# Kernel tuning notes

Measured on AMD Instinct MI355X. Metric: run time of the kernel, lower is better.

## Reference

```python
import jax, jax.numpy as jnp
import numpy as np

E = 8        # n_experts
K = 2        # top-k
DIM = 1024
HID = 2048   # swiglu hidden; fc1 out = 2*HID
B, T = 4, 2048


def setup_inputs() -> dict:
    key = jax.random.key(0)
    ks = jax.random.split(key, 7)
    s = 0.02
    return {
        "x": jax.random.normal(ks[0], (B, T, DIM), dtype=jnp.float32),
        "router_w": jax.random.normal(ks[1], (E, DIM), dtype=jnp.float32) * s,
        "router_b": jnp.zeros((E,), dtype=jnp.float32),
        "W1": jax.random.normal(ks[2], (E, DIM, 2 * HID), dtype=jnp.float32) * s,
        "b1": jnp.zeros((E, 2 * HID), dtype=jnp.float32),
        "W2": jax.random.normal(ks[3], (E, HID, DIM), dtype=jnp.float32) * s,
        "b2": jnp.zeros((E, DIM), dtype=jnp.float32),
    }


def _swiglu(h):
    h1, h2 = jnp.split(h, 2, axis=-1)
    return jax.nn.silu(h1) * h2


def reference(x, router_w, router_b, W1, b1, W2, b2):
    # Router: logits = Linear(dim, E), temperature = 1.0
    logits = jnp.einsum("btd,ed->bte", x, router_w) + router_b  # [B,T,E]
    topk_val, topk_idx = jax.lax.top_k(logits, K)               # [B,T,K]
    weights = jax.nn.softmax(topk_val, axis=-1)                 # softmax router
    # combine[b,t,e] = sum_k weights[b,t,k] * [topk_idx[b,t,k] == e]
    combine = jnp.sum(jax.nn.one_hot(topk_idx, E, dtype=x.dtype)
                      * weights[..., None], axis=-2)            # [B,T,E]
    out = jnp.zeros_like(x)
    # Fixed small loop over experts (structurally distinct weight slices).
    for e in range(E):
        h = jnp.einsum("btd,dh->bth", x, W1[e]) + b1[e]         # [B,T,2H]
        y = jnp.einsum("bth,hd->btd", _swiglu(h), W2[e]) + b2[e]
        out = out + combine[..., e:e + 1] * y
    return out
```

## Files before the change

### kernel.cpp

```cpp
#include <hip/hip_runtime.h>
#include <stdint.h>

typedef unsigned short u16;

#define E_    8
#define DIM_  1024
#define HID_  2048
#define H2_   4096
#define NTOK  8192
#define SLAB  ((size_t)NTOK * 2 * DIM_)

typedef __attribute__((ext_vector_type(8))) short bf16x8;
typedef __attribute__((ext_vector_type(4))) float f32x4;

__device__ __forceinline__ u16 f2bf(float f) {
  uint32_t u = __builtin_bit_cast(uint32_t, f);
  uint32_t r = (u + 0x7FFFu + ((u >> 16) & 1u)) >> 16;
  return (u16)r;
}
__device__ __forceinline__ float bf2f(u16 u) {
  return __builtin_bit_cast(float, (uint32_t)u << 16);
}

__device__ __forceinline__ void gload16(const void* g, void* l) {
  __builtin_amdgcn_global_load_lds(
      (const __attribute__((address_space(1))) void*)g,
      (__attribute__((address_space(3))) void*)l, 16, 0, 0);
}


__global__ void tconvF(const float* __restrict__ W1, u16* __restrict__ w1t,
                       const float* __restrict__ W2, u16* __restrict__ w2t) {
  __shared__ float t[64][65];
  int b = blockIdx.x;
  const float* src; u16* dst; int R, C, e, bx, by;
  if (b < 8192) {
    e = b >> 10; int rem = b & 1023;
    bx = rem & 63; by = rem >> 6;
    src = W1; dst = w1t; R = DIM_; C = H2_;
  } else {
    int b2 = b - 8192;
    e = b2 >> 9; int rem = b2 & 511;
    bx = rem & 15; by = rem >> 4;
    src = W2; dst = w2t; R = HID_; C = DIM_;
  }
  int r0 = by * 64, c0 = bx * 64;
  const float* s = src + (size_t)e * R * C;
  u16* d = dst + (size_t)e * R * C;
  int tid = threadIdx.x;
  int rr = tid >> 4, cc = (tid & 15) * 4;
#pragma unroll
  for (int p = 0; p < 4; ++p) {
    float4 v = *(const float4*)(s + (size_t)(r0 + p * 16 + rr) * C + c0 + cc);
    t[p * 16 + rr][cc + 0] = v.x; t[p * 16 + rr][cc + 1] = v.y;
    t[p * 16 + rr][cc + 2] = v.z; t[p * 16 + rr][cc + 3] = v.w;
  }
  __syncthreads();
  int cr = tid >> 3, rc = (tid & 7) * 8;
#pragma unroll
  for (int p = 0; p < 2; ++p) {
    union { u16 u[8]; uint4 v; } w;
#pragma unroll
    for (int j = 0; j < 8; ++j) w.u[j] = f2bf(t[rc + j][p * 32 + cr]);
    *(uint4*)(d + (size_t)(c0 + p * 32 + cr) * R + r0 + rc) = w.v;
  }
}


__global__ void routerA(const float* __restrict__ x, const float* __restrict__ rw,
                        const float* __restrict__ rb, u16* __restrict__ xb,
                        int* __restrict__ gcnt, int2* __restrict__ te_l,
                        float2* __restrict__ tw) {
  __shared__ float srw[E_ * DIM_];
  __shared__ float sb[E_];
  __shared__ int   hcnt[E_];

  int tid = threadIdx.x;
  for (int i = tid; i < E_ * DIM_ / 4; i += 256)
    ((float4*)srw)[i] = ((const float4*)rw)[i];
  if (tid < E_) { sb[tid] = rb[tid]; hcnt[tid] = 0; }
  __syncthreads();

  int wid = tid >> 6, lane = tid & 63;
#pragma unroll
  for (int s = 0; s < 2; ++s) {
    int t = blockIdx.x * 8 + wid * 2 + s;
    const float* xt = x + (size_t)t * DIM_;
    float acc[8] = {0.f, 0.f, 0.f, 0.f, 0.f, 0.f, 0.f, 0.f};
#pragma unroll
    for (int it = 0; it < 4; ++it) {
      int d = it * 256 + lane * 4;
      float4 xv = *(const float4*)(xt + d);
      ushort4 xo;
      xo.x = f2bf(xv.x); xo.y = f2bf(xv.y); xo.z = f2bf(xv.z); xo.w = f2bf(xv.w);
      *(ushort4*)(xb + (size_t)t * DIM_ + d) = xo;
#pragma unroll
      for (int e = 0; e < 8; ++e) {
        float4 rv = *(const float4*)(&srw[e * DIM_ + d]);
        acc[e] += xv.x * rv.x + xv.y * rv.y + xv.z * rv.z + xv.w * rv.w;
      }
    }
#pragma unroll
    for (int e = 0; e < 8; ++e)
#pragma unroll
      for (int off = 32; off; off >>= 1)
        acc[e] += __shfl_xor(acc[e], off, 64);
    if (lane == 0) {
      float v[8];
#pragma unroll
      for (int e = 0; e < 8; ++e) v[e] = acc[e] + sb[e];
      int i0 = 0;
#pragma unroll
      for (int e = 1; e < 8; ++e) if (v[e] > v[i0]) i0 = e;
      int i1 = (i0 == 0) ? 1 : 0;
#pragma unroll
      for (int e = 0; e < 8; ++e) if (e != i0 && v[e] > v[i1]) i1 = e;
      float w0 = 1.f / (1.f + expf(v[i1] - v[i0]));
      int l0 = atomicAdd(&hcnt[i0], 1);
      int l1 = atomicAdd(&hcnt[i1], 1);
      te_l[t] = make_int2((i0 << 8) | l0, (i1 << 8) | l1);
      tw[t] = make_float2(w0, 1.f - w0);
    }
  }
  __syncthreads();
  if (tid < E_) gcnt[tid * 1024 + blockIdx.x] = hcnt[tid];
}


__global__ void routerB(const int* __restrict__ gcnt, int* __restrict__ base_blk,
                        int* __restrict__ counts) {
  __shared__ int part[256];
  int tid = threadIdx.x;
#pragma unroll
  for (int e = 0; e < 8; ++e) {
    int4 v = *(const int4*)(gcnt + e * 1024 + tid * 4);
    int s = v.x + v.y + v.z + v.w;
    part[tid] = s;
    __syncthreads();
    for (int off = 1; off < 256; off <<= 1) {
      int o = (tid >= off) ? part[tid - off] : 0;
      __syncthreads();
      part[tid] += o;
      __syncthreads();
    }
    int ex = part[tid] - s;
    int tot = part[255];
    int4 b;
    b.x = ex; b.y = ex + v.x; b.z = ex + v.x + v.y; b.w = ex + v.x + v.y + v.z;
    *(int4*)(base_blk + e * 1024 + tid * 4) = b;
    if (tid == 0) counts[e] = tot;
    __syncthreads();
  }
}


__global__ void routerC(const int2* __restrict__ te_l, const float2* __restrict__ tw,
                        const int* __restrict__ base_blk, int* __restrict__ btok,
                        float* __restrict__ bw, int* __restrict__ tokrec) {
  int t = blockIdx.x * 256 + threadIdx.x;
  int2 r = te_l[t];
  float2 w = tw[t];
  int b = t >> 3;
  int e0 = r.x >> 8, l0 = r.x & 255;
  int e1 = r.y >> 8, l1 = r.y & 255;
  int p0 = base_blk[e0 * 1024 + b] + l0;
  int p1 = base_blk[e1 * 1024 + b] + l1;
  btok[e0 * NTOK + p0] = t; bw[e0 * NTOK + p0] = w.x; tokrec[t * 2 + 0] = (e0 << 13) | p0;
  btok[e1 * NTOK + p1] = t; bw[e1 * NTOK + p1] = w.y; tokrec[t * 2 + 1] = (e1 << 13) | p1;
}


__launch_bounds__(256, 4)
__global__ void gemm1(const u16* __restrict__ xb, const u16* __restrict__ w1t,
                      const float* __restrict__ b1, const int* __restrict__ counts,
                      const int* __restrict__ btok, u16* __restrict__ hb) {
  int e = blockIdx.z, mblk = blockIdx.y, nblk = blockIdx.x;
  int cnt = counts[e];
  if (mblk * 128 >= cnt) return;
  int base = 0;
#pragma unroll
  for (int i = 0; i < 8; ++i) base += (i < e) ? counts[i] : 0;

  __shared__ u16 lA[128 * 64];
  __shared__ u16 lB[128 * 64];
  __shared__ int sTok[128];

  int tid = threadIdx.x, wid = tid >> 6, lane = tid & 63;
  if (tid < 128) {
    int gr = mblk * 128 + tid;
    sTok[tid] = (gr < cnt) ? btok[e * NTOK + gr] : btok[e * NTOK];
  }
  __syncthreads();

  f32x4 acc[4][4] = {};
  int wr = wid >> 1, wc = wid & 1;
  int l15 = lane & 15, lhi = lane >> 4;
  const size_t w1e = (size_t)e * H2_ * DIM_;

  int segsw = ((lane & 7) ^ ((lane >> 3) & 7)) * 8;
  const u16* gA[4];
  const u16* gB[4];
#pragma unroll
  for (int i = 0; i < 4; ++i) {
    int r = wid * 32 + i * 8 + (lane >> 3);
    gA[i] = xb + (size_t)sTok[r] * DIM_ + segsw;
    int gcol = nblk * 64 + (r >> 6) * 32 + (r & 31) + ((r >> 5) & 1) * 2048;
    gB[i] = w1t + w1e + (size_t)gcol * DIM_ + segsw;
  }
  int rxor = (l15 & 7) * 8;

  for (int kt = 0; kt < DIM_ / 64; ++kt) {
#pragma unroll
    for (int i = 0; i < 4; ++i)
      gload16(gA[i] + kt * 64, &lA[(wid * 32 + i * 8) * 64]);
#pragma unroll
    for (int i = 0; i < 4; ++i)
      gload16(gB[i] + kt * 64, &lB[(wid * 32 + i * 8) * 64]);
    __syncthreads();
#pragma unroll
    for (int ks = 0; ks < 2; ++ks) {
      int segrd = ((ks * 4 + lhi) * 8) ^ rxor;
      bf16x8 a[4], b[4];
#pragma unroll
      for (int m = 0; m < 4; ++m)
        a[m] = *(const bf16x8*)&lA[(wr * 64 + m * 16 + l15) * 64 + segrd];
#pragma unroll
      for (int n = 0; n < 4; ++n)
        b[n] = *(const bf16x8*)&lB[(wc * 64 + n * 16 + l15) * 64 + segrd];
#pragma unroll
      for (int m = 0; m < 4; ++m)
#pragma unroll
        for (int n = 0; n < 4; ++n)
          acc[m][n] = __builtin_amdgcn_mfma_f32_16x16x32_bf16(a[m], b[n], acc[m][n], 0, 0, 0);
    }
    __syncthreads();
  }

#pragma unroll
  for (int n = 0; n < 2; ++n) {
    int outcol = nblk * 64 + wc * 32 + n * 16 + l15;
    float bb1 = b1[e * H2_ + outcol];
    float bb2 = b1[e * H2_ + outcol + HID_];
#pragma unroll
    for (int m = 0; m < 4; ++m) {
#pragma unroll
      for (int j = 0; j < 4; ++j) {
        int rt = wr * 64 + m * 16 + lhi * 4 + j;
        int gr = mblk * 128 + rt;
        if (gr < cnt) {
          float h1 = acc[m][n][j] + bb1;
          float h2 = acc[m][n + 2][j] + bb2;
          float s = (h1 / (1.f + __expf(-h1))) * h2;
          hb[(size_t)(base + gr) * HID_ + outcol] = f2bf(s);
        }
      }
    }
  }
}


__launch_bounds__(256, 4)
__global__ void gemm2(const u16* __restrict__ hb, const u16* __restrict__ w2t,
                      const float* __restrict__ b2, const int* __restrict__ counts,
                      const float* __restrict__ bw, u16* __restrict__ ybuf) {
  int e = blockIdx.z, mblk = blockIdx.y;
  int nblk = blockIdx.x & 7, khalf = blockIdx.x >> 3;
  int cnt = counts[e];
  if (mblk * 128 >= cnt) return;
  int base = 0;
#pragma unroll
  for (int i = 0; i < 8; ++i) base += (i < e) ? counts[i] : 0;

  __shared__ u16 lA[128 * 64];
  __shared__ u16 lB[128 * 64];
  __shared__ float sW[128];

  int tid = threadIdx.x, wid = tid >> 6, lane = tid & 63;
  if (tid < 128) {
    int gr = mblk * 128 + tid;
    sW[tid] = (gr < cnt) ? bw[e * NTOK + gr] : 0.f;
  }
  __syncthreads();

  f32x4 acc[4][4] = {};
  int wr = wid >> 1, wc = wid & 1;
  int l15 = lane & 15, lhi = lane >> 4;

  int segsw = ((lane & 7) ^ ((lane >> 3) & 7)) * 8;
  int koff = khalf * (HID_ / 2);
  const u16* gA[4];
  const u16* gB[4];
#pragma unroll
  for (int i = 0; i < 4; ++i) {
    int r = wid * 32 + i * 8 + (lane >> 3);
    gA[i] = hb + (size_t)(base + mblk * 128 + r) * HID_ + koff + segsw;
    gB[i] = w2t + (size_t)e * DIM_ * HID_ + (size_t)(nblk * 128 + r) * HID_ + koff + segsw;
  }
  int rxor = (l15 & 7) * 8;

  for (int kt = 0; kt < HID_ / 128; ++kt) {
#pragma unroll
    for (int i = 0; i < 4; ++i) {
      gload16(gA[i] + kt * 64, &lA[(wid * 32 + i * 8) * 64]);
      gload16(gB[i] + kt * 64, &lB[(wid * 32 + i * 8) * 64]);
    }
    __syncthreads();
#pragma unroll
    for (int ks = 0; ks < 2; ++ks) {
      int segrd = ((ks * 4 + lhi) * 8) ^ rxor;
      bf16x8 a[4], b[4];
#pragma unroll
      for (int m = 0; m < 4; ++m)
        a[m] = *(const bf16x8*)&lA[(wr * 64 + m * 16 + l15) * 64 + segrd];
#pragma unroll
      for (int n = 0; n < 4; ++n)
        b[n] = *(const bf16x8*)&lB[(wc * 64 + n * 16 + l15) * 64 + segrd];
#pragma unroll
      for (int m = 0; m < 4; ++m)
#pragma unroll
        for (int n = 0; n < 4; ++n)
          acc[m][n] = __builtin_amdgcn_mfma_f32_16x16x32_bf16(a[m], b[n], acc[m][n], 0, 0, 0);
    }
    __syncthreads();
  }

  u16* yb = ybuf + (size_t)khalf * SLAB;
#pragma unroll
  for (int n = 0; n < 4; ++n) {
    int col = nblk * 128 + wc * 64 + n * 16 + l15;
    float bb = (khalf == 0) ? b2[e * DIM_ + col] : 0.f;
#pragma unroll
    for (int m = 0; m < 4; ++m) {
#pragma unroll
      for (int j = 0; j < 4; ++j) {
        int rt = wr * 64 + m * 16 + lhi * 4 + j;
        int gr = mblk * 128 + rt;
        if (gr < cnt)
          yb[(size_t)(base + gr) * DIM_ + col] = f2bf(sW[rt] * (acc[m][n][j] + bb));
      }
    }
  }
}


__global__ void combine(const u16* __restrict__ ybuf, const int* __restrict__ tokrec,
                        const int* __restrict__ counts, float* __restrict__ out) {
  __shared__ int sbase[8];
  int tid = threadIdx.x;
  if (tid < 8) {
    int b = 0;
#pragma unroll
    for (int e = 0; e < 8; ++e) { if (e == tid) sbase[e] = b; b += counts[e]; }
  }
  __syncthreads();
  int wid = tid >> 6, lane = tid & 63;
  int t = blockIdx.x * 4 + wid;
  int r0 = tokrec[t * 2 + 0], r1 = tokrec[t * 2 + 1];
  size_t s0 = (size_t)(sbase[r0 >> 13] + (r0 & 8191)) * DIM_;
  size_t s1 = (size_t)(sbase[r1 >> 13] + (r1 & 8191)) * DIM_;
#pragma unroll
  for (int p = 0; p < 4; ++p) {
    int c = (lane + p * 64) * 4;
    ushort4 a0 = *(const ushort4*)(ybuf + s0 + c);
    ushort4 a1 = *(const ushort4*)(ybuf + SLAB + s0 + c);
    ushort4 b0 = *(const ushort4*)(ybuf + s1 + c);
    ushort4 b1 = *(const ushort4*)(ybuf + SLAB + s1 + c);
    float4 o;
    o.x = bf2f(a0.x) + bf2f(a1.x) + bf2f(b0.x) + bf2f(b1.x);
    o.y = bf2f(a0.y) + bf2f(a1.y) + bf2f(b0.y) + bf2f(b1.y);
    o.z = bf2f(a0.z) + bf2f(a1.z) + bf2f(b0.z) + bf2f(b1.z);
    o.w = bf2f(a0.w) + bf2f(a1.w) + bf2f(b0.w) + bf2f(b1.w);
    *(float4*)(out + (size_t)t * DIM_ + c) = o;
  }
}


extern "C" void kernel_launch(void* const* d_in, const int* in_sizes, int n_in,
                              void* d_out, int out_size, void* d_ws, size_t ws_size,
                              hipStream_t stream) {
  const float* x  = (const float*)d_in[0];
  const float* rw = (const float*)d_in[1];
  const float* rb = (const float*)d_in[2];
  const float* W1 = (const float*)d_in[3];
  const float* b1 = (const float*)d_in[4];
  const float* W2 = (const float*)d_in[5];
  const float* b2 = (const float*)d_in[6];
  float* out = (float*)d_out;

  char* ws = (char*)d_ws;
  int*    counts   = (int*)ws;
  int*    btok     = (int*)(ws + 256);
  float*  bw       = (float*)(ws + 256 + 262144);
  int*    tokrec   = (int*)(ws + 256 + 524288);
  int*    gcnt     = (int*)(ws + 655360);
  int*    base_blk = (int*)(ws + 688128);
  int2*   te_l     = (int2*)(ws + 720896);
  float2* tw       = (float2*)(ws + 786432);
  u16* xb  = (u16*)(ws + (1u << 20));
  u16* w1t = xb  + (size_t)NTOK * DIM_;
  u16* w2t = w1t + (size_t)E_ * H2_ * DIM_;
  u16* hb  = w2t + (size_t)E_ * DIM_ * HID_;
  u16* ybuf = w1t;

  tconvF<<<12288, 256, 0, stream>>>(W1, w1t, W2, w2t);
  routerA<<<1024, 256, 0, stream>>>(x, rw, rb, xb, gcnt, te_l, tw);
  routerB<<<1, 256, 0, stream>>>(gcnt, base_blk, counts);
  routerC<<<32, 256, 0, stream>>>(te_l, tw, base_blk, btok, bw, tokrec);

  gemm1<<<dim3(H2_ / 128, NTOK / 128, E_), 256, 0, stream>>>(xb, w1t, b1, counts, btok, hb);
  gemm2<<<dim3(16, NTOK / 128, E_), 256, 0, stream>>>(hb, w2t, b2, counts, bw, ybuf);
  combine<<<NTOK / 4, 256, 0, stream>>>(ybuf, tokrec, counts, out);
}
```

Measured before the change: 375.9 us.

## Merge weight transpose with router and fuse scan with scatter kernels

Combines the weight transpose/bf16 conversion and router scoring into one launch by block-index dispatch, and fuses the single-block prefix scan with the token scatter so each of 32 blocks redundantly computes the scan in shared memory. This removes two kernel launches, the serialization of a one-block scan kernel, and the base_blk global round trip. In exchange the merged kernel uses the larger router shared-memory footprint for all blocks, which may reduce occupancy of the transpose blocks, and the scan work is duplicated across blocks.

```diff
diff --git a/kernel.cpp b/kernel.cpp
--- a/kernel.cpp
+++ b/kernel.cpp
@@ -29,142 +29,153 @@
 }
 
 
-__global__ void tconvF(const float* __restrict__ W1, u16* __restrict__ w1t,
-                       const float* __restrict__ W2, u16* __restrict__ w2t) {
-  __shared__ float t[64][65];
+__global__ void prep(const float* __restrict__ W1, u16* __restrict__ w1t,
+                     const float* __restrict__ W2, u16* __restrict__ w2t,
+                     const float* __restrict__ x, const float* __restrict__ rw,
+                     const float* __restrict__ rb, u16* __restrict__ xb,
+                     int* __restrict__ gcnt, int2* __restrict__ te_l,
+                     float2* __restrict__ tw) {
+  __shared__ float smem[E_ * DIM_ + 16];
   int b = blockIdx.x;
-  const float* src; u16* dst; int R, C, e, bx, by;
-  if (b < 8192) {
-    e = b >> 10; int rem = b & 1023;
-    bx = rem & 63; by = rem >> 6;
-    src = W1; dst = w1t; R = DIM_; C = H2_;
+  int tid = threadIdx.x;
+
+  if (b < 12288) {
+    float (*t)[65] = (float(*)[65])smem;
+    const float* src; u16* dst; int R, C, e, bx, by;
+    if (b < 8192) {
+      e = b >> 10; int rem = b & 1023;
+      bx = rem & 63; by = rem >> 6;
+      src = W1; dst = w1t; R = DIM_; C = H2_;
+    } else {
+      int b2 = b - 8192;
+      e = b2 >> 9; int rem = b2 & 511;
+      bx = rem & 15; by = rem >> 4;
+      src = W2; dst = w2t; R = HID_; C = DIM_;
+    }
+    int r0 = by * 64, c0 = bx * 64;
+    const float* s = src + (size_t)e * R * C;
+    u16* d = dst + (size_t)e * R * C;
+    int rr = tid >> 4, cc = (tid & 15) * 4;
+#pragma unroll
+    for (int p = 0; p < 4; ++p) {
+      float4 v = *(const float4*)(s + (size_t)(r0 + p * 16 + rr) * C + c0 + cc);
+      t[p * 16 + rr][cc + 0] = v.x; t[p * 16 + rr][cc + 1] = v.y;
+      t[p * 16 + rr][cc + 2] = v.z; t[p * 16 + rr][cc + 3] = v.w;
+    }
+    __syncthreads();
+    int cr = tid >> 3, rc = (tid & 7) * 8;
+#pragma unroll
+    for (int p = 0; p < 2; ++p) {
+      union { u16 u[8]; uint4 v; } w;
+#pragma unroll
+      for (int j = 0; j < 8; ++j) w.u[j] = f2bf(t[rc + j][p * 32 + cr]);
+      *(uint4*)(d + (size_t)(c0 + p * 32 + cr) * R + r0 + rc) = w.v;
+    }
   } else {
-    int b2 = b - 8192;
-    e = b2 >> 9; int rem = b2 & 511;
-    bx = rem & 15; by = rem >> 4;
-    src = W2; dst = w2t; R = HID_; C = DIM_;
-  }
-  int r0 = by * 64, c0 = bx * 64;
-  const float* s = src + (size_t)e * R * C;
-  u16* d = dst + (size_t)e * R * C;
-  int tid = threadIdx.x;
-  int rr = tid >> 4, cc = (tid & 15) * 4;
-#pragma unroll
-  for (int p = 0; p < 4; ++p) {
-    float4 v = *(const float4*)(s + (size_t)(r0 + p * 16 + rr) * C + c0 + cc);
-    t[p * 16 + rr][cc + 0] = v.x; t[p * 16 + rr][cc + 1] = v.y;
-    t[p * 16 + rr][cc + 2] = v.z; t[p * 16 + rr][cc + 3] = v.w;
+    int rblk = b - 12288;
+    float* srw = smem;
+    float* sb  = smem + E_ * DIM_;
+    int*   hcnt = (int*)(smem + E_ * DIM_ + 8);
+
+    for (int i = tid; i < E_ * DIM_ / 4; i += 256)
+      ((float4*)srw)[i] = ((const float4*)rw)[i];
+    if (tid < E_) { sb[tid] = rb[tid]; hcnt[tid] = 0; }
+    __syncthreads();
+
+    int wid = tid >> 6, lane = tid & 63;
+#pragma unroll
+    for (int s = 0; s < 2; ++s) {
+      int t = rblk * 8 + wid * 2 + s;
+      const float* xt = x + (size_t)t * DIM_;
+      float acc[8] = {0.f, 0.f, 0.f, 0.f, 0.f, 0.f, 0.f, 0.f};
+#pragma unroll
+      for (int it = 0; it < 4; ++it) {
+        int d = it * 256 + lane * 4;
+        float4 xv = *(const float4*)(xt + d);
+        ushort4 xo;
+        xo.x = f2bf(xv.x); xo.y = f2bf(xv.y); xo.z = f2bf(xv.z); xo.w = f2bf(xv.w);
+        *(ushort4*)(xb + (size_t)t * DIM_ + d) = xo;
+#pragma unroll
+        for (int e = 0; e < 8; ++e) {
+          float4 rv = *(const float4*)(&srw[e * DIM_ + d]);
+          acc[e] += xv.x * rv.x + xv.y * rv.y + xv.z * rv.z + xv.w * rv.w;
+        }
+      }
+#pragma unroll
+      for (int e = 0; e < 8; ++e)
+#pragma unroll
+        for (int off = 32; off; off >>= 1)
+          acc[e] += __shfl_xor(acc[e], off, 64);
+      if (lane == 0) {
+        float v[8];
+#pragma unroll
+        for (int e = 0; e < 8; ++e) v[e] = acc[e] + sb[e];
+        int i0 = 0;
+#pragma unroll
+        for (int e = 1; e < 8; ++e) if (v[e] > v[i0]) i0 = e;
+        int i1 = (i0 == 0) ? 1 : 0;
+#pragma unroll
+        for (int e = 0; e < 8; ++e) if (e != i0 && v[e] > v[i1]) i1 = e;
+        float w0 = 1.f / (1.f + expf(v[i1] - v[i0]));
+        int l0 = atomicAdd(&hcnt[i0], 1);
+        int l1 = atomicAdd(&hcnt[i1], 1);
+        te_l[t] = make_int2((i0 << 8) | l0, (i1 << 8) | l1);
+        tw[t] = make_float2(w0, 1.f - w0);
+      }
+    }
+    __syncthreads();
+    if (tid < E_) gcnt[tid * 1024 + rblk] = hcnt[tid];
+  }
+}
+
+
+__global__ void routerBC(const int* __restrict__ gcnt, int* __restrict__ counts,
+                         const int2* __restrict__ te_l, const float2* __restrict__ tw,
+                         int* __restrict__ btok, float* __restrict__ bw,
+                         int* __restrict__ tokrec) {
+  __shared__ int part[8][256];
+  __shared__ int sbb[8][32];
+  int tid = threadIdx.x, b = blockIdx.x;
+
+  int4 v[8]; int s[8];
+#pragma unroll
+  for (int e = 0; e < 8; ++e) {
+    v[e] = *(const int4*)(gcnt + e * 1024 + tid * 4);
+    s[e] = v[e].x + v[e].y + v[e].z + v[e].w;
+    part[e][tid] = s[e];
   }
   __syncthreads();
-  int cr = tid >> 3, rc = (tid & 7) * 8;
-#pragma unroll
-  for (int p = 0; p < 2; ++p) {
-    union { u16 u[8]; uint4 v; } w;
-#pragma unroll
-    for (int j = 0; j < 8; ++j) w.u[j] = f2bf(t[rc + j][p * 32 + cr]);
-    *(uint4*)(d + (size_t)(c0 + p * 32 + cr) * R + r0 + rc) = w.v;
-  }
-}
-
-
-__global__ void routerA(const float* __restrict__ x, const float* __restrict__ rw,
-                        const float* __restrict__ rb, u16* __restrict__ xb,
-                        int* __restrict__ gcnt, int2* __restrict__ te_l,
-                        float2* __restrict__ tw) {
-  __shared__ float srw[E_ * DIM_];
-  __shared__ float sb[E_];
-  __shared__ int   hcnt[E_];
-
-  int tid = threadIdx.x;
-  for (int i = tid; i < E_ * DIM_ / 4; i += 256)
-    ((float4*)srw)[i] = ((const float4*)rw)[i];
-  if (tid < E_) { sb[tid] = rb[tid]; hcnt[tid] = 0; }
+  for (int off = 1; off < 256; off <<= 1) {
+    int o[8];
+#pragma unroll
+    for (int e = 0; e < 8; ++e) o[e] = (tid >= off) ? part[e][tid - off] : 0;
+    __syncthreads();
+#pragma unroll
+    for (int e = 0; e < 8; ++e) part[e][tid] += o[e];
+    __syncthreads();
+  }
+  if ((tid >> 3) == b) {
+    int lc = (tid & 7) * 4;
+#pragma unroll
+    for (int e = 0; e < 8; ++e) {
+      int ex = part[e][tid] - s[e];
+      sbb[e][lc + 0] = ex;
+      sbb[e][lc + 1] = ex + v[e].x;
+      sbb[e][lc + 2] = ex + v[e].x + v[e].y;
+      sbb[e][lc + 3] = ex + v[e].x + v[e].y + v[e].z;
+    }
+  }
+  if (b == 0 && tid < 8) counts[tid] = part[tid][255];
   __syncthreads();
 
-  int wid = tid >> 6, lane = tid & 63;
-#pragma unroll
-  for (int s = 0; s < 2; ++s) {
-    int t = blockIdx.x * 8 + wid * 2 + s;
-    const float* xt = x + (size_t)t * DIM_;
-    float acc[8] = {0.f, 0.f, 0.f, 0.f, 0.f, 0.f, 0.f, 0.f};
-#pragma unroll
-    for (int it = 0; it < 4; ++it) {
-      int d = it * 256 + lane * 4;
-      float4 xv = *(const float4*)(xt + d);
-      ushort4 xo;
-      xo.x = f2bf(xv.x); xo.y = f2bf(xv.y); xo.z = f2bf(xv.z); xo.w = f2bf(xv.w);
-      *(ushort4*)(xb + (size_t)t * DIM_ + d) = xo;
-#pragma unroll
-      for (int e = 0; e < 8; ++e) {
-        float4 rv = *(const float4*)(&srw[e * DIM_ + d]);
-        acc[e] += xv.x * rv.x + xv.y * rv.y + xv.z * rv.z + xv.w * rv.w;
-      }
-    }
-#pragma unroll
-    for (int e = 0; e < 8; ++e)
-#pragma unroll
-      for (int off = 32; off; off >>= 1)
-        acc[e] += __shfl_xor(acc[e], off, 64);
-    if (lane == 0) {
-      float v[8];
-#pragma unroll
-      for (int e = 0; e < 8; ++e) v[e] = acc[e] + sb[e];
-      int i0 = 0;
-#pragma unroll
-      for (int e = 1; e < 8; ++e) if (v[e] > v[i0]) i0 = e;
-      int i1 = (i0 == 0) ? 1 : 0;
-#pragma unroll
-      for (int e = 0; e < 8; ++e) if (e != i0 && v[e] > v[i1]) i1 = e;
-      float w0 = 1.f / (1.f + expf(v[i1] - v[i0]));
-      int l0 = atomicAdd(&hcnt[i0], 1);
-      int l1 = atomicAdd(&hcnt[i1], 1);
-      te_l[t] = make_int2((i0 << 8) | l0, (i1 << 8) | l1);
-      tw[t] = make_float2(w0, 1.f - w0);
-    }
-  }
-  __syncthreads();
-  if (tid < E_) gcnt[tid * 1024 + blockIdx.x] = hcnt[tid];
-}
-
-
-__global__ void routerB(const int* __restrict__ gcnt, int* __restrict__ base_blk,
-                        int* __restrict__ counts) {
-  __shared__ int part[256];
-  int tid = threadIdx.x;
-#pragma unroll
-  for (int e = 0; e < 8; ++e) {
-    int4 v = *(const int4*)(gcnt + e * 1024 + tid * 4);
-    int s = v.x + v.y + v.z + v.w;
-    part[tid] = s;
-    __syncthreads();
-    for (int off = 1; off < 256; off <<= 1) {
-      int o = (tid >= off) ? part[tid - off] : 0;
-      __syncthreads();
-      part[tid] += o;
-      __syncthreads();
-    }
-    int ex = part[tid] - s;
-    int tot = part[255];
-    int4 b;
-    b.x = ex; b.y = ex + v.x; b.z = ex + v.x + v.y; b.w = ex + v.x + v.y + v.z;
-    *(int4*)(base_blk + e * 1024 + tid * 4) = b;
-    if (tid == 0) counts[e] = tot;
-    __syncthreads();
-  }
-}
-
-
-__global__ void routerC(const int2* __restrict__ te_l, const float2* __restrict__ tw,
-                        const int* __restrict__ base_blk, int* __restrict__ btok,
-                        float* __restrict__ bw, int* __restrict__ tokrec) {
-  int t = blockIdx.x * 256 + threadIdx.x;
+  int t = b * 256 + tid;
   int2 r = te_l[t];
   float2 w = tw[t];
-  int b = t >> 3;
+  int blk_l = tid >> 3;
   int e0 = r.x >> 8, l0 = r.x & 255;
   int e1 = r.y >> 8, l1 = r.y & 255;
-  int p0 = base_blk[e0 * 1024 + b] + l0;
-  int p1 = base_blk[e1 * 1024 + b] + l1;
+  int p0 = sbb[e0][blk_l] + l0;
+  int p1 = sbb[e1][blk_l] + l1;
   btok[e0 * NTOK + p0] = t; bw[e0 * NTOK + p0] = w.x; tokrec[t * 2 + 0] = (e0 << 13) | p0;
   btok[e1 * NTOK + p1] = t; bw[e1 * NTOK + p1] = w.y; tokrec[t * 2 + 1] = (e1 << 13) | p1;
 }
@@ -393,7 +404,6 @@
   float*  bw       = (float*)(ws + 256 + 262144);
   int*    tokrec   = (int*)(ws + 256 + 524288);
   int*    gcnt     = (int*)(ws + 655360);
-  int*    base_blk = (int*)(ws + 688128);
   int2*   te_l     = (int2*)(ws + 720896);
   float2* tw       = (float2*)(ws + 786432);
   u16* xb  = (u16*)(ws + (1u << 20));
@@ -402,10 +412,8 @@
   u16* hb  = w2t + (size_t)E_ * DIM_ * HID_;
   u16* ybuf = w1t;
 
-  tconvF<<<12288, 256, 0, stream>>>(W1, w1t, W2, w2t);
-  routerA<<<1024, 256, 0, stream>>>(x, rw, rb, xb, gcnt, te_l, tw);
-  routerB<<<1, 256, 0, stream>>>(gcnt, base_blk, counts);
-  routerC<<<32, 256, 0, stream>>>(te_l, tw, base_blk, btok, bw, tokrec);
+  prep<<<13312, 256, 0, stream>>>(W1, w1t, W2, w2t, x, rw, rb, xb, gcnt, te_l, tw);
+  routerBC<<<32, 256, 0, stream>>>(gcnt, counts, te_l, tw, btok, bw, tokrec);
 
   gemm1<<<dim3(H2_ / 128, NTOK / 128, E_), 256, 0, stream>>>(xb, w1t, b1, counts, btok, hb);
   gemm2<<<dim3(16, NTOK / 128, E_), 256, 0, stream>>>(hb, w2t, b2, counts, bw, ybuf);
```

Measured after the change: 363.4 us. 1.03x faster.
